# Performance work log

Measured on AMD Instinct MI355X. Metric: run time of the kernel, lower is better.

The kernel has to match this reference:

```python
import itertools
import jax, jax.numpy as jnp
import numpy as np

# ---- constant tables / bases ----
Y_TABLE_NP = np.array([
    [16, 11, 10, 16, 24, 40, 51, 61],
    [12, 12, 14, 19, 26, 58, 60, 55],
    [14, 13, 16, 24, 40, 57, 69, 56],
    [14, 17, 22, 29, 51, 87, 80, 62],
    [18, 22, 37, 56, 68, 109, 103, 77],
    [24, 35, 55, 64, 81, 104, 113, 92],
    [49, 64, 78, 87, 103, 121, 120, 101],
    [72, 92, 95, 98, 112, 100, 103, 99]], dtype=np.float32)
C_TABLE_NP = np.full((8, 8), 99, dtype=np.float32)
C_TABLE_NP[:4, :4] = np.array([[17, 18, 24, 47], [18, 21, 26, 66],
                               [24, 26, 56, 99], [47, 66, 99, 99]], dtype=np.float32)

def _bases():
    dct = np.zeros((8, 8, 8, 8), dtype=np.float32)
    idct = np.zeros((8, 8, 8, 8), dtype=np.float32)
    for x, y, u, v in itertools.product(range(8), repeat=4):
        dct[x, y, u, v] = np.cos((2 * x + 1) * u * np.pi / 16) * np.cos((2 * y + 1) * v * np.pi / 16)
        idct[x, y, u, v] = np.cos((2 * u + 1) * x * np.pi / 16) * np.cos((2 * v + 1) * y * np.pi / 16)
    alpha = np.array([1.0 / np.sqrt(2)] + [1.0] * 7, dtype=np.float32)
    ao = np.outer(alpha, alpha).astype(np.float32)
    return jnp.asarray(dct), jnp.asarray(ao * 0.25), jnp.asarray(idct), jnp.asarray(ao)

DCT_T, DCT_SCALE, IDCT_T, ALPHA = _bases()
FACTOR = 0.4  # quality_to_factor(80) = (200 - 2*80)/100


def diff_round(x):
    r = jnp.round(x)
    return r + (x - r) ** 3


def _blocks(img):  # (B,H,W) -> (B, H*W/64, 8, 8)
    B, H, W = img.shape
    return img.reshape(B, H // 8, 8, W // 8, 8).transpose(0, 1, 3, 2, 4).reshape(B, -1, 8, 8)


def _merge(patches, H, W):  # (B, N, 8, 8) -> (B, H, W)
    B = patches.shape[0]
    return patches.reshape(B, H // 8, W // 8, 8, 8).transpose(0, 1, 3, 2, 4).reshape(B, H, W)


def setup_inputs() -> dict:
    key = jax.random.key(0)
    image = jax.random.uniform(key, (32, 3, 512, 512), dtype=jnp.float32)
    return {"image": image,
            "y_table": jnp.asarray(Y_TABLE_NP),
            "c_table": jnp.asarray(C_TABLE_NP)}


def reference(image, y_table, c_table):
    B, _, H, W = image.shape
    x = image * 255.0
    # RGB -> YCbCr (matrix stored transposed in torch, tensordot over channel)
    rgb2ycc = jnp.array([[0.299, 0.587, 0.114],
                         [-0.168736, -0.331264, 0.5],
                         [0.5, -0.418688, -0.081312]], dtype=jnp.float32)
    shift = jnp.array([0.0, 128.0, 128.0], dtype=jnp.float32)
    ycc = jnp.einsum('bchw,kc->bhwk', x, rgb2ycc) + shift  # (B,H,W,3)
    y = ycc[..., 0]
    # chroma subsampling: 2x2 average pool
    def pool2(ch):
        return ch.reshape(B, H // 2, 2, W // 2, 2).mean(axis=(2, 4))
    cb = pool2(ycc[..., 1])
    cr = pool2(ycc[..., 2])

    def compress(ch, table):
        blk = _blocks(ch) - 128.0
        d = DCT_SCALE * jnp.einsum('bnxy,xyuv->bnuv', blk, DCT_T)
        return diff_round(d / (table * FACTOR))

    yq = compress(y, y_table)
    cbq = compress(cb, c_table)
    crq = compress(cr, c_table)

    def decompress(q, table, h, w):
        d = (q * (table * FACTOR)) * ALPHA
        blk = 0.25 * jnp.einsum('bnuv,uvxy->bnxy', d, IDCT_T) + 128.0
        return _merge(blk, h, w)

    y_rec = decompress(yq, y_table, H, W)
    cb_rec = decompress(cbq, c_table, H // 2, W // 2)
    cr_rec = decompress(crq, c_table, H // 2, W // 2)

    def up2(ch):
        b, h, w = ch.shape
        return jnp.broadcast_to(ch[:, :, None, :, None], (b, h, 2, w, 2)).reshape(b, 2 * h, 2 * w)

    ycc_rec = jnp.stack([y_rec, up2(cb_rec), up2(cr_rec)], axis=-1)  # (B,H,W,3)
    ycc2rgb = jnp.array([[1.0, 0.0, 1.402],
                         [1.0, -0.344136, -0.714136],
                         [1.0, 1.772, 0.0]], dtype=jnp.float32)
    shift2 = jnp.array([0.0, -128.0, -128.0], dtype=jnp.float32)
    rgb = jnp.einsum('bhwk,ck->bhwc', ycc_rec + shift2, ycc2rgb)
    rgb = rgb.transpose(0, 3, 1, 2)  # (B,3,H,W)
    return jnp.clip(rgb, 0.0, 255.0) / 255.0
```

## Files before the change

### kernel.cpp

```cpp
#include <hip/hip_runtime.h>
#include <math.h>

#define IMG_H 512
#define IMG_W 512
#define IMG_HW (IMG_H * IMG_W)

namespace {

constexpr float CFv[9] = {
    1.0f,
    0.98078528040323044913f,
    0.92387953251128675613f,
    0.83146961230254523708f,
    0.70710678118654752440f,
    0.55557023301960222474f,
    0.38268343236508977173f,
    0.19509032201612826785f,
    0.0f
};

struct CTab {
    float  cf[8][8];
    double cd[8][8];
    float  aof[8][8];
    float  scalef[8][8];
};

constexpr CTab make_ctab() {
    CTab t{};
    for (int y = 0; y < 8; y++) {
        for (int v = 0; v < 8; v++) {
            int a = ((2 * y + 1) * v) & 31;
            if (a > 16) a = 32 - a;
            float val = (a <= 8) ? CFv[a] : -CFv[16 - a];
            t.cf[y][v] = val;
            t.cd[y][v] = (double)val;
        }
    }
    constexpr float A0 = 0.70710678118654752440f;
    for (int u = 0; u < 8; u++) {
        for (int v = 0; v < 8; v++) {
            float au = (u == 0) ? A0 : 1.0f;
            float av = (v == 0) ? A0 : 1.0f;
            float ao = au * av;
            t.aof[u][v] = ao;
            t.scalef[u][v] = ao * 0.25f;
        }
    }
    return t;
}

constexpr CTab CT = make_ctab();

__device__ __forceinline__ void fwd8_d(const double a[8], double s[8]) {
    double e0 = a[0] + a[7], e1 = a[1] + a[6], e2 = a[2] + a[5], e3 = a[3] + a[4];
    double o0 = a[0] - a[7], o1 = a[1] - a[6], o2 = a[2] - a[5], o3 = a[3] - a[4];
    double ee0 = e0 + e3, ee1 = e1 + e2, eo0 = e0 - e3, eo1 = e1 - e2;
    s[0] = ee0 + ee1;
    s[4] = (ee0 - ee1) * CT.cd[0][4];
    s[2] = eo0 * CT.cd[0][2] + eo1 * CT.cd[1][2];
    s[6] = eo0 * CT.cd[0][6] + eo1 * CT.cd[1][6];
    #pragma unroll
    for (int k = 0; k < 4; k++) {
        const int v = 2 * k + 1;
        s[v] = o0 * CT.cd[0][v] + o1 * CT.cd[1][v] + o2 * CT.cd[2][v] + o3 * CT.cd[3][v];
    }
}

__device__ __forceinline__ void inv8_f(const float d[8], float m[8]) {
    float eea = fmaf(CT.cf[0][4], d[4], d[0]);
    float eeb = fmaf(CT.cf[1][4], d[4], d[0]);
    float u2a = d[2] * CT.cf[0][2] + d[6] * CT.cf[0][6];
    float u2b = d[2] * CT.cf[1][2] + d[6] * CT.cf[1][6];
    float E0 = eea + u2a, E1 = eeb + u2b, E2 = eeb - u2b, E3 = eea - u2a;
    float O0 = d[1] * CT.cf[0][1] + d[3] * CT.cf[0][3] + d[5] * CT.cf[0][5] + d[7] * CT.cf[0][7];
    float O1 = d[1] * CT.cf[1][1] + d[3] * CT.cf[1][3] + d[5] * CT.cf[1][5] + d[7] * CT.cf[1][7];
    float O2 = d[1] * CT.cf[2][1] + d[3] * CT.cf[2][3] + d[5] * CT.cf[2][5] + d[7] * CT.cf[2][7];
    float O3 = d[1] * CT.cf[3][1] + d[3] * CT.cf[3][3] + d[5] * CT.cf[3][5] + d[7] * CT.cf[3][7];
    m[0] = E0 + O0; m[7] = E0 - O0;
    m[1] = E1 + O1; m[6] = E1 - O1;
    m[2] = E2 + O2; m[5] = E2 - O2;
    m[3] = E3 + O3; m[4] = E3 - O3;
}

}

#define WAVE_BYTES 3584
#define OFF_CBP 2304
#define OFF_CRP 2944
#define OFF_CBR 1280
#define OFF_CRR 1664
#define OFF_QYF 14336
#define OFF_QCF 14976
#define OFF_DSY 15616
#define OFF_DSC 16000
#define SMEM_BYTES 16384

__global__ void __launch_bounds__(256, 8) djpeg_kernel(
    const float* __restrict__ img,
    const float* __restrict__ ytab,
    const float* __restrict__ ctab,
    float* __restrict__ out)
{
    __shared__ __align__(16) unsigned char smem[SMEM_BYTES];
    const int t = threadIdx.x;
    const int w = t >> 6, l = t & 63;
    unsigned char* wb = smem + w * WAVE_BYTES;
    double* lYd = (double*)wb;
    double* cbP = (double*)(wb + OFF_CBP);
    double* crP = (double*)(wb + OFF_CRP);
    float*  yR  = (float*)wb;
    float*  cbR = (float*)(wb + OFF_CBR);
    float*  crR = (float*)(wb + OFF_CRR);
    double* qYfs = (double*)(smem + OFF_QYF);
    double* qCfs = (double*)(smem + OFF_QCF);
    float*  dsY  = (float*)(smem + OFF_DSY);
    float*  dsC  = (float*)(smem + OFF_DSC);

    const int bi = blockIdx.z;
    const int X0 = blockIdx.x * 64 + w * 16;
    const int Y0 = blockIdx.y * 16;
    const int q = l & 3, row = l >> 2;

    const size_t base = ((size_t)bi * 3) * IMG_HW + (size_t)(Y0 + row) * IMG_W + X0 + q * 4;
    const float4 rf = *(const float4*)(img + base);
    const float4 gf = *(const float4*)(img + base + IMG_HW);
    const float4 bf = *(const float4*)(img + base + 2 * IMG_HW);

    if (t < 128) {
        const float* tab = (t < 64) ? ytab : ctab;
        double* qf = (t < 64) ? qYfs : qCfs;
        float*  df = (t < 64) ? dsY : dsC;
        int e = t & 63, u = e >> 3, v = e & 7;
        float tfacf = tab[e] * 0.4f;
        double tf = (double)tfacf;
        qf[v * 10 + u] = (double)CT.scalef[u][v] / tf;
        df[v * 12 + u] = (float)(tf * (double)CT.aof[u][v]);
    }
    __syncthreads();

    {
        const double kYR =  (double)0.299f    * 255.0, kYG =  (double)0.587f    * 255.0, kYB =  (double)0.114f    * 255.0;
        const double kbR = -(double)0.168736f * 255.0, kbG = -(double)0.331264f * 255.0, kbB =  (double)0.5f      * 255.0;
        const double krR =  (double)0.5f      * 255.0, krG = -(double)0.418688f * 255.0, krB = -(double)0.081312f * 255.0;
        const float rr[4] = {rf.x, rf.y, rf.z, rf.w};
        const float gg[4] = {gf.x, gf.y, gf.z, gf.w};
        const float bb[4] = {bf.x, bf.y, bf.z, bf.w};
        double Yv[4];
        double cb0 = 0.0, cb1 = 0.0, cr0 = 0.0, cr1 = 0.0;
        #pragma unroll
        for (int i = 0; i < 4; i++) {
            double R = (double)rr[i], G = (double)gg[i], B = (double)bb[i];
            Yv[i] = kYR * R + kYG * G + kYB * B;
            double Cb = kbR * R + kbG * G + kbB * B + 128.0;
            double Cr = krR * R + krG * G + krB * B + 128.0;
            if (i < 2) { cb0 += Cb; cr0 += Cr; } else { cb1 += Cb; cr1 += Cr; }
        }
        double2* yw = (double2*)(lYd + row * 18 + q * 4);
        yw[0] = make_double2(Yv[0], Yv[1]);
        yw[1] = make_double2(Yv[2], Yv[3]);
        cb0 += __shfl_xor(cb0, 4);
        cb1 += __shfl_xor(cb1, 4);
        cr0 += __shfl_xor(cr0, 4);
        cr1 += __shfl_xor(cr1, 4);
        if ((row & 1) == 0) {
            const int pr = row >> 1;
            *(double2*)(cbP + pr * 10 + q * 2) = make_double2(cb0 * 0.25, cb1 * 0.25);
            *(double2*)(crP + pr * 10 + q * 2) = make_double2(cr0 * 0.25, cr1 * 0.25);
        }
    }
    asm volatile("s_waitcnt lgkmcnt(0)" ::: "memory");

    const int g = l >> 3, r = l & 7;
    double* blkd = lYd;  float* blkf = yR;
    const double* qfp = qYfs;  const float* dfp = dsY;
    int sD = 18, sF = 20;
    if (g < 4) {
        const int by = g >> 1, bx = g & 1;
        blkd = lYd + by * 144 + bx * 8;
        blkf = yR  + by * 160 + bx * 8;
    } else {
        blkd = (g == 5) ? crP : cbP;
        blkf = (g == 5) ? crR : cbR;
        qfp = qCfs; dfp = dsC;
        sD = 10; sF = 12;
    }

    if (g < 6) {
        const double* sp = blkd + r * sD;
        const double2 a01 = *(const double2*)(sp + 0);
        const double2 a23 = *(const double2*)(sp + 2);
        const double2 a45 = *(const double2*)(sp + 4);
        const double2 a67 = *(const double2*)(sp + 6);
        const double a[8] = {a01.x, a01.y, a23.x, a23.y, a45.x, a45.y, a67.x, a67.y};
        double s1[8];
        fwd8_d(a, s1);
        s1[0] -= 1024.0;

        #pragma unroll
        for (int v = 0; v < 8; v++) blkd[v * sD + r] = s1[v];
        asm volatile("s_waitcnt lgkmcnt(0)" ::: "memory");
        const double* rp = blkd + r * sD;
        const double2 b01 = *(const double2*)(rp + 0);
        const double2 b23 = *(const double2*)(rp + 2);
        const double2 b45 = *(const double2*)(rp + 4);
        const double2 b67 = *(const double2*)(rp + 6);
        const double s2[8] = {b01.x, b01.y, b23.x, b23.y, b45.x, b45.y, b67.x, b67.y};

        double D[8];
        fwd8_d(s2, D);
        const double2 f01 = *(const double2*)(qfp + r * 10 + 0);
        const double2 f23 = *(const double2*)(qfp + r * 10 + 2);
        const double2 f45 = *(const double2*)(qfp + r * 10 + 4);
        const double2 f67 = *(const double2*)(qfp + r * 10 + 6);
        const double fsv[8] = {f01.x, f01.y, f23.x, f23.y, f45.x, f45.y, f67.x, f67.y};
        const float4 dA = *(const float4*)(dfp + r * 12);
        const float4 dB = *(const float4*)(dfp + r * 12 + 4);
        const float dsv[8] = {dA.x, dA.y, dA.z, dA.w, dB.x, dB.y, dB.z, dB.w};
        float dq[8];
        #pragma unroll
        for (int u = 0; u < 8; u++) {
            double xq = D[u] * fsv[u];
            double rq = rint(xq);
            float ef  = (float)(xq - rq);
            float rqf = (float)rq;
            dq[u] = (rqf + ef * ef * ef) * dsv[u];
        }

        float mc[8];
        inv8_f(dq, mc);

        #pragma unroll
        for (int p = 0; p < 8; p++) blkf[p * sF + r] = mc[p];
        asm volatile("s_waitcnt lgkmcnt(0)" ::: "memory");
        const float* fp_ = blkf + r * sF;
        const float4 m0 = *(const float4*)(fp_);
        const float4 m1 = *(const float4*)(fp_ + 4);
        const float mrow[8] = {m0.x, m0.y, m0.z, m0.w, m1.x, m1.y, m1.z, m1.w};

        float px[8];
        inv8_f(mrow, px);
        float* fw = blkf + r * sF;
        *(float4*)(fw)     = make_float4(fmaf(0.25f, px[0], 128.0f), fmaf(0.25f, px[1], 128.0f),
                                         fmaf(0.25f, px[2], 128.0f), fmaf(0.25f, px[3], 128.0f));
        *(float4*)(fw + 4) = make_float4(fmaf(0.25f, px[4], 128.0f), fmaf(0.25f, px[5], 128.0f),
                                         fmaf(0.25f, px[6], 128.0f), fmaf(0.25f, px[7], 128.0f));
    }
    asm volatile("s_waitcnt lgkmcnt(0)" ::: "memory");

    {
        const float4 yv  = *(const float4*)(yR + row * 20 + q * 4);
        const float2 cbv = *(const float2*)(cbR + (row >> 1) * 12 + q * 2);
        const float2 crv = *(const float2*)(crR + (row >> 1) * 12 + q * 2);
        const float yy[4]  = {yv.x, yv.y, yv.z, yv.w};
        const float cbs[2] = {cbv.x - 128.0f, cbv.y - 128.0f};
        const float crs[2] = {crv.x - 128.0f, crv.y - 128.0f};
        float R4[4], G4[4], B4[4];
        #pragma unroll
        for (int i = 0; i < 4; i++) {
            float Yv = yy[i], Cb = cbs[i >> 1], Cr = crs[i >> 1];
            float Rr = Yv + 1.402f * Cr;
            float Gg = Yv - 0.344136f * Cb - 0.714136f * Cr;
            float Bb = Yv + 1.772f * Cb;
            R4[i] = fminf(fmaxf(Rr, 0.0f), 255.0f) * (1.0f / 255.0f);
            G4[i] = fminf(fmaxf(Gg, 0.0f), 255.0f) * (1.0f / 255.0f);
            B4[i] = fminf(fmaxf(Bb, 0.0f), 255.0f) * (1.0f / 255.0f);
        }
        *(float4*)(out + base)              = make_float4(R4[0], R4[1], R4[2], R4[3]);
        *(float4*)(out + base + IMG_HW)     = make_float4(G4[0], G4[1], G4[2], G4[3]);
        *(float4*)(out + base + 2 * IMG_HW) = make_float4(B4[0], B4[1], B4[2], B4[3]);
    }
}

extern "C" void kernel_launch(void* const* d_in, const int* in_sizes, int n_in,
                              void* d_out, int out_size, void* d_ws, size_t ws_size,
                              hipStream_t stream) {
    (void)n_in; (void)out_size; (void)d_ws; (void)ws_size;
    const float* img = (const float*)d_in[0];
    const float* yt  = (const float*)d_in[1];
    const float* ct  = (const float*)d_in[2];
    float* out = (float*)d_out;
    int B = in_sizes[0] / (3 * IMG_HW);
    dim3 grid(IMG_W / 64, IMG_H / 16, B);
    djpeg_kernel<<<grid, dim3(256, 1, 1), 0, stream>>>(img, yt, ct, out);
}
```

Measured before the change: 185.7 us.

## Replace LDS block transposes with register shuffles and per-row pixel mapping

Remaps each wave so every lane owns one row of an 8x8 block, loading 8 pixels per lane directly. The four LDS store/reload transposes (forward DCT, inverse DCT, chroma and colour staging) become butterfly __shfl_xor transposes and __shfl gathers. Shared memory drops to the quantisation tables only, which removes LDS traffic and may allow more blocks per CU. In exchange only half the lanes load and store global memory, which may hurt coalescing, and many double-precision shuffles are added.

After: 198.0 us. 1.07x slower.

```diff
diff --git a/kernel.cpp b/kernel.cpp
--- a/kernel.cpp
+++ b/kernel.cpp
@@ -83,18 +83,47 @@
     m[3] = E3 + O3; m[4] = E3 - O3;
 }
 
-}
-
-#define WAVE_BYTES 3584
-#define OFF_CBP 2304
-#define OFF_CRP 2944
-#define OFF_CBR 1280
-#define OFF_CRR 1664
-#define OFF_QYF 14336
-#define OFF_QCF 14976
-#define OFF_DSY 15616
-#define OFF_DSC 16000
-#define SMEM_BYTES 16384
+__device__ __forceinline__ void xpose8_d(double v[8]) {
+    const int l = threadIdx.x & 7;
+    #pragma unroll
+    for (int m = 1; m < 8; m <<= 1) {
+        #pragma unroll
+        for (int k = 0; k < 8; k++) {
+            if ((k & m) == 0) {
+                const int kp = k | m;
+                double send = (l & m) ? v[k] : v[kp];
+                double recv = __shfl_xor(send, m);
+                v[k]  = (l & m) ? recv : v[k];
+                v[kp] = (l & m) ? v[kp] : recv;
+            }
+        }
+    }
+}
+
+__device__ __forceinline__ void xpose8_f(float v[8]) {
+    const int l = threadIdx.x & 7;
+    #pragma unroll
+    for (int m = 1; m < 8; m <<= 1) {
+        #pragma unroll
+        for (int k = 0; k < 8; k++) {
+            if ((k & m) == 0) {
+                const int kp = k | m;
+                float send = (l & m) ? v[k] : v[kp];
+                float recv = __shfl_xor(send, m);
+                v[k]  = (l & m) ? recv : v[k];
+                v[kp] = (l & m) ? v[kp] : recv;
+            }
+        }
+    }
+}
+
+}
+
+#define OFF_QYF 0
+#define OFF_QCF 640
+#define OFF_DSY 1280
+#define OFF_DSC 1664
+#define SMEM_BYTES 2048
 
 __global__ void __launch_bounds__(256, 8) djpeg_kernel(
     const float* __restrict__ img,
@@ -103,29 +132,32 @@
     float* __restrict__ out)
 {
     __shared__ __align__(16) unsigned char smem[SMEM_BYTES];
-    const int t = threadIdx.x;
-    const int w = t >> 6, l = t & 63;
-    unsigned char* wb = smem + w * WAVE_BYTES;
-    double* lYd = (double*)wb;
-    double* cbP = (double*)(wb + OFF_CBP);
-    double* crP = (double*)(wb + OFF_CRP);
-    float*  yR  = (float*)wb;
-    float*  cbR = (float*)(wb + OFF_CBR);
-    float*  crR = (float*)(wb + OFF_CRR);
     double* qYfs = (double*)(smem + OFF_QYF);
     double* qCfs = (double*)(smem + OFF_QCF);
     float*  dsY  = (float*)(smem + OFF_DSY);
     float*  dsC  = (float*)(smem + OFF_DSC);
 
+    const int t = threadIdx.x;
+    const int w = t >> 6, l = t & 63;
+    const int g = l >> 3, r = l & 7;
+
     const int bi = blockIdx.z;
     const int X0 = blockIdx.x * 64 + w * 16;
     const int Y0 = blockIdx.y * 16;
-    const int q = l & 3, row = l >> 2;
-
-    const size_t base = ((size_t)bi * 3) * IMG_HW + (size_t)(Y0 + row) * IMG_W + X0 + q * 4;
-    const float4 rf = *(const float4*)(img + base);
-    const float4 gf = *(const float4*)(img + base + IMG_HW);
-    const float4 bf = *(const float4*)(img + base + 2 * IMG_HW);
+
+    const int pr = (g >> 1) * 8 + r;
+    const int pc = (g & 1) * 8;
+    const size_t pbase = ((size_t)bi * 3) * IMG_HW + (size_t)(Y0 + pr) * IMG_W + X0 + pc;
+
+    float4 rf0, rf1, gf0, gf1, bf0, bf1;
+    if (l < 32) {
+        rf0 = *(const float4*)(img + pbase);
+        rf1 = *(const float4*)(img + pbase + 4);
+        gf0 = *(const float4*)(img + pbase + IMG_HW);
+        gf1 = *(const float4*)(img + pbase + IMG_HW + 4);
+        bf0 = *(const float4*)(img + pbase + 2 * IMG_HW);
+        bf1 = *(const float4*)(img + pbase + 2 * IMG_HW + 4);
+    }
 
     if (t < 128) {
         const float* tab = (t < 64) ? ytab : ctab;
@@ -139,136 +171,127 @@
     }
     __syncthreads();
 
-    {
+    double a[8]  = {0.0, 0.0, 0.0, 0.0, 0.0, 0.0, 0.0, 0.0};
+    double vb[4] = {0.0, 0.0, 0.0, 0.0};
+    double vr[4] = {0.0, 0.0, 0.0, 0.0};
+    if (l < 32) {
         const double kYR =  (double)0.299f    * 255.0, kYG =  (double)0.587f    * 255.0, kYB =  (double)0.114f    * 255.0;
         const double kbR = -(double)0.168736f * 255.0, kbG = -(double)0.331264f * 255.0, kbB =  (double)0.5f      * 255.0;
         const double krR =  (double)0.5f      * 255.0, krG = -(double)0.418688f * 255.0, krB = -(double)0.081312f * 255.0;
-        const float rr[4] = {rf.x, rf.y, rf.z, rf.w};
-        const float gg[4] = {gf.x, gf.y, gf.z, gf.w};
-        const float bb[4] = {bf.x, bf.y, bf.z, bf.w};
-        double Yv[4];
-        double cb0 = 0.0, cb1 = 0.0, cr0 = 0.0, cr1 = 0.0;
-        #pragma unroll
-        for (int i = 0; i < 4; i++) {
-            double R = (double)rr[i], G = (double)gg[i], B = (double)bb[i];
-            Yv[i] = kYR * R + kYG * G + kYB * B;
-            double Cb = kbR * R + kbG * G + kbB * B + 128.0;
-            double Cr = krR * R + krG * G + krB * B + 128.0;
-            if (i < 2) { cb0 += Cb; cr0 += Cr; } else { cb1 += Cb; cr1 += Cr; }
-        }
-        double2* yw = (double2*)(lYd + row * 18 + q * 4);
-        yw[0] = make_double2(Yv[0], Yv[1]);
-        yw[1] = make_double2(Yv[2], Yv[3]);
-        cb0 += __shfl_xor(cb0, 4);
-        cb1 += __shfl_xor(cb1, 4);
-        cr0 += __shfl_xor(cr0, 4);
-        cr1 += __shfl_xor(cr1, 4);
-        if ((row & 1) == 0) {
-            const int pr = row >> 1;
-            *(double2*)(cbP + pr * 10 + q * 2) = make_double2(cb0 * 0.25, cb1 * 0.25);
-            *(double2*)(crP + pr * 10 + q * 2) = make_double2(cr0 * 0.25, cr1 * 0.25);
-        }
-    }
-    asm volatile("s_waitcnt lgkmcnt(0)" ::: "memory");
-
-    const int g = l >> 3, r = l & 7;
-    double* blkd = lYd;  float* blkf = yR;
-    const double* qfp = qYfs;  const float* dfp = dsY;
-    int sD = 18, sF = 20;
-    if (g < 4) {
-        const int by = g >> 1, bx = g & 1;
-        blkd = lYd + by * 144 + bx * 8;
-        blkf = yR  + by * 160 + bx * 8;
-    } else {
-        blkd = (g == 5) ? crP : cbP;
-        blkf = (g == 5) ? crR : cbR;
-        qfp = qCfs; dfp = dsC;
-        sD = 10; sF = 12;
-    }
-
-    if (g < 6) {
-        const double* sp = blkd + r * sD;
-        const double2 a01 = *(const double2*)(sp + 0);
-        const double2 a23 = *(const double2*)(sp + 2);
-        const double2 a45 = *(const double2*)(sp + 4);
-        const double2 a67 = *(const double2*)(sp + 6);
-        const double a[8] = {a01.x, a01.y, a23.x, a23.y, a45.x, a45.y, a67.x, a67.y};
-        double s1[8];
-        fwd8_d(a, s1);
-        s1[0] -= 1024.0;
-
-        #pragma unroll
-        for (int v = 0; v < 8; v++) blkd[v * sD + r] = s1[v];
-        asm volatile("s_waitcnt lgkmcnt(0)" ::: "memory");
-        const double* rp = blkd + r * sD;
-        const double2 b01 = *(const double2*)(rp + 0);
-        const double2 b23 = *(const double2*)(rp + 2);
-        const double2 b45 = *(const double2*)(rp + 4);
-        const double2 b67 = *(const double2*)(rp + 6);
-        const double s2[8] = {b01.x, b01.y, b23.x, b23.y, b45.x, b45.y, b67.x, b67.y};
-
-        double D[8];
-        fwd8_d(s2, D);
-        const double2 f01 = *(const double2*)(qfp + r * 10 + 0);
-        const double2 f23 = *(const double2*)(qfp + r * 10 + 2);
-        const double2 f45 = *(const double2*)(qfp + r * 10 + 4);
-        const double2 f67 = *(const double2*)(qfp + r * 10 + 6);
-        const double fsv[8] = {f01.x, f01.y, f23.x, f23.y, f45.x, f45.y, f67.x, f67.y};
-        const float4 dA = *(const float4*)(dfp + r * 12);
-        const float4 dB = *(const float4*)(dfp + r * 12 + 4);
-        const float dsv[8] = {dA.x, dA.y, dA.z, dA.w, dB.x, dB.y, dB.z, dB.w};
-        float dq[8];
-        #pragma unroll
-        for (int u = 0; u < 8; u++) {
-            double xq = D[u] * fsv[u];
-            double rq = rint(xq);
-            float ef  = (float)(xq - rq);
-            float rqf = (float)rq;
-            dq[u] = (rqf + ef * ef * ef) * dsv[u];
-        }
-
-        float mc[8];
-        inv8_f(dq, mc);
-
-        #pragma unroll
-        for (int p = 0; p < 8; p++) blkf[p * sF + r] = mc[p];
-        asm volatile("s_waitcnt lgkmcnt(0)" ::: "memory");
-        const float* fp_ = blkf + r * sF;
-        const float4 m0 = *(const float4*)(fp_);
-        const float4 m1 = *(const float4*)(fp_ + 4);
-        const float mrow[8] = {m0.x, m0.y, m0.z, m0.w, m1.x, m1.y, m1.z, m1.w};
-
-        float px[8];
-        inv8_f(mrow, px);
-        float* fw = blkf + r * sF;
-        *(float4*)(fw)     = make_float4(fmaf(0.25f, px[0], 128.0f), fmaf(0.25f, px[1], 128.0f),
-                                         fmaf(0.25f, px[2], 128.0f), fmaf(0.25f, px[3], 128.0f));
-        *(float4*)(fw + 4) = make_float4(fmaf(0.25f, px[4], 128.0f), fmaf(0.25f, px[5], 128.0f),
-                                         fmaf(0.25f, px[6], 128.0f), fmaf(0.25f, px[7], 128.0f));
-    }
-    asm volatile("s_waitcnt lgkmcnt(0)" ::: "memory");
+        const float rr_[8] = {rf0.x, rf0.y, rf0.z, rf0.w, rf1.x, rf1.y, rf1.z, rf1.w};
+        const float gg_[8] = {gf0.x, gf0.y, gf0.z, gf0.w, gf1.x, gf1.y, gf1.z, gf1.w};
+        const float bb_[8] = {bf0.x, bf0.y, bf0.z, bf0.w, bf1.x, bf1.y, bf1.z, bf1.w};
+        #pragma unroll
+        for (int k = 0; k < 4; k++) {
+            double cbp = 0.0, crp = 0.0;
+            #pragma unroll
+            for (int h = 0; h < 2; h++) {
+                const int j = 2 * k + h;
+                double R = (double)rr_[j], G = (double)gg_[j], B = (double)bb_[j];
+                a[j] = kYR * R + kYG * G + kYB * B;
+                double Cb = kbR * R + kbG * G + kbB * B + 128.0;
+                double Cr = krR * R + krG * G + krB * B + 128.0;
+                cbp += Cb;
+                crp += Cr;
+            }
+            vb[k] = (cbp + __shfl_xor(cbp, 1)) * 0.25;
+            vr[k] = (crp + __shfl_xor(crp, 1)) * 0.25;
+        }
+    }
 
     {
-        const float4 yv  = *(const float4*)(yR + row * 20 + q * 4);
-        const float2 cbv = *(const float2*)(cbR + (row >> 1) * 12 + q * 2);
-        const float2 crv = *(const float2*)(crR + (row >> 1) * 12 + q * 2);
-        const float yy[4]  = {yv.x, yv.y, yv.z, yv.w};
-        const float cbs[2] = {cbv.x - 128.0f, cbv.y - 128.0f};
-        const float crs[2] = {crv.x - 128.0f, crv.y - 128.0f};
-        float R4[4], G4[4], B4[4];
-        #pragma unroll
-        for (int i = 0; i < 4; i++) {
-            float Yv = yy[i], Cb = cbs[i >> 1], Cr = crs[i >> 1];
-            float Rr = Yv + 1.402f * Cr;
-            float Gg = Yv - 0.344136f * Cb - 0.714136f * Cr;
-            float Bb = Yv + 1.772f * Cb;
-            R4[i] = fminf(fmaxf(Rr, 0.0f), 255.0f) * (1.0f / 255.0f);
-            G4[i] = fminf(fmaxf(Gg, 0.0f), 255.0f) * (1.0f / 255.0f);
-            B4[i] = fminf(fmaxf(Bb, 0.0f), 255.0f) * (1.0f / 255.0f);
-        }
-        *(float4*)(out + base)              = make_float4(R4[0], R4[1], R4[2], R4[3]);
-        *(float4*)(out + base + IMG_HW)     = make_float4(G4[0], G4[1], G4[2], G4[3]);
-        *(float4*)(out + base + 2 * IMG_HW) = make_float4(B4[0], B4[1], B4[2], B4[3]);
+        const int rr2  = (l - 32) & 7;
+        const int srcA = ((rr2 >> 2) * 16) + 2 * (rr2 & 3);
+        const int srcB = srcA + 8;
+        double ga[8];
+        #pragma unroll
+        for (int k = 0; k < 4; k++) {
+            double bA = __shfl(vb[k], srcA);
+            double bB = __shfl(vb[k], srcB);
+            double rA = __shfl(vr[k], srcA);
+            double rB = __shfl(vr[k], srcB);
+            const bool isCr = (l >= 40);
+            ga[k]     = isCr ? rA : bA;
+            ga[4 + k] = isCr ? rB : bB;
+        }
+        if (g >= 4) {
+            #pragma unroll
+            for (int k = 0; k < 8; k++) a[k] = ga[k];
+        }
+    }
+
+    double s1[8];
+    fwd8_d(a, s1);
+    s1[0] -= 1024.0;
+    xpose8_d(s1);
+    double D[8];
+    fwd8_d(s1, D);
+
+    const double* qfp = (g < 4) ? qYfs : qCfs;
+    const float*  dfp = (g < 4) ? dsY : dsC;
+    const double2 f01 = *(const double2*)(qfp + r * 10 + 0);
+    const double2 f23 = *(const double2*)(qfp + r * 10 + 2);
+    const double2 f45 = *(const double2*)(qfp + r * 10 + 4);
+    const double2 f67 = *(const double2*)(qfp + r * 10 + 6);
+    const double fsv[8] = {f01.x, f01.y, f23.x, f23.y, f45.x, f45.y, f67.x, f67.y};
+    const float4 dA = *(const float4*)(dfp + r * 12);
+    const float4 dB = *(const float4*)(dfp + r * 12 + 4);
+    const float dsv[8] = {dA.x, dA.y, dA.z, dA.w, dB.x, dB.y, dB.z, dB.w};
+    float dq[8];
+    #pragma unroll
+    for (int u = 0; u < 8; u++) {
+        double xq = D[u] * fsv[u];
+        double rq = rint(xq);
+        float ef  = (float)(xq - rq);
+        float rqf = (float)rq;
+        dq[u] = (rqf + ef * ef * ef) * dsv[u];
+    }
+
+    float mc[8];
+    inv8_f(dq, mc);
+    xpose8_f(mc);
+    float px[8];
+    inv8_f(mc, px);
+    #pragma unroll
+    for (int j = 0; j < 8; j++) px[j] = fmaf(0.25f, px[j], 128.0f);
+
+    {
+        const int rrY = (g >> 1) * 4 + (r >> 1);
+        const int sCb = 32 + rrY, sCr = 40 + rrY;
+        float cbU[4], crU[4];
+        #pragma unroll
+        for (int k = 0; k < 4; k++) {
+            float lo = __shfl(px[k], sCb);
+            float hi = __shfl(px[4 + k], sCb);
+            cbU[k] = (g & 1) ? hi : lo;
+            lo = __shfl(px[k], sCr);
+            hi = __shfl(px[4 + k], sCr);
+            crU[k] = (g & 1) ? hi : lo;
+        }
+        if (l < 32) {
+            float R8[8], G8[8], B8[8];
+            #pragma unroll
+            for (int j = 0; j < 8; j++) {
+                float Yv = px[j];
+                float Cb = cbU[j >> 1] - 128.0f;
+                float Cr = crU[j >> 1] - 128.0f;
+                float Rr = Yv + 1.402f * Cr;
+                float Gg = Yv - 0.344136f * Cb - 0.714136f * Cr;
+                float Bb = Yv + 1.772f * Cb;
+                R8[j] = fminf(fmaxf(Rr, 0.0f), 255.0f) * (1.0f / 255.0f);
+                G8[j] = fminf(fmaxf(Gg, 0.0f), 255.0f) * (1.0f / 255.0f);
+                B8[j] = fminf(fmaxf(Bb, 0.0f), 255.0f) * (1.0f / 255.0f);
+            }
+            float* o0 = out + pbase;
+            float* o1 = out + pbase + IMG_HW;
+            float* o2 = out + pbase + 2 * IMG_HW;
+            *(float4*)(o0)     = make_float4(R8[0], R8[1], R8[2], R8[3]);
+            *(float4*)(o0 + 4) = make_float4(R8[4], R8[5], R8[6], R8[7]);
+            *(float4*)(o1)     = make_float4(G8[0], G8[1], G8[2], G8[3]);
+            *(float4*)(o1 + 4) = make_float4(G8[4], G8[5], G8[6], G8[7]);
+            *(float4*)(o2)     = make_float4(B8[0], B8[1], B8[2], B8[3]);
+            *(float4*)(o2 + 4) = make_float4(B8[4], B8[5], B8[6], B8[7]);
+        }
     }
 }
 
```
